# Optimization experiments

Hardware: AMD Instinct MI355X
Metric: run time of the kernel (lower is better)

## Reference

```python
import jax, jax.numpy as jnp
import numpy as np

N_NODES = 50000


def setup_inputs() -> dict:
    key = jax.random.key(0)
    ks = jax.random.split(key, 9)
    d = 256
    E = 800000
    inp = {
        "x": jax.random.normal(ks[0], (N_NODES, d), dtype=jnp.float32),
        "edge_index": jax.random.randint(ks[1], (2, E), 0, N_NODES, dtype=jnp.int64),
    }
    # 3 GCNConv layers, each: weight [in, out] and bias [out] (Glorot-ish scale)
    scale = 1.0 / np.sqrt(d)
    for i in range(3):
        inp[f"W{i+1}"] = jax.random.normal(ks[2 + 2 * i], (d, d), dtype=jnp.float32) * scale
        inp[f"b{i+1}"] = jnp.zeros((d,), dtype=jnp.float32)
    return inp


def _gcn_conv(h, src, dst, norm, W, b, n_nodes):
    # linear transform then normalized gather-scatter aggregation
    h = h @ W                                   # [N, out]
    msg = h[src] * norm[:, None]                # [E+N, out]
    out = jax.ops.segment_sum(msg, dst, num_segments=n_nodes)
    return out + b


def reference(x, edge_index, W1, b1, W2, b2, W3, b3):
    n = x.shape[0]
    loop = jnp.arange(n, dtype=edge_index.dtype)
    src = jnp.concatenate([edge_index[0], loop])  # add self-loops
    dst = jnp.concatenate([edge_index[1], loop])
    # symmetric normalization: deg^{-1/2}[src] * deg^{-1/2}[dst]
    deg = jax.ops.segment_sum(jnp.ones_like(dst, dtype=x.dtype), dst, num_segments=n)
    dinv = jnp.where(deg > 0, jax.lax.rsqrt(deg), 0.0)
    norm = dinv[src] * dinv[dst]

    h = _gcn_conv(x, src, dst, norm, W1, b1, n)
    h = jax.nn.relu(h)
    h = _gcn_conv(h, src, dst, norm, W2, b2, n)
    h = jax.nn.relu(h)
    h = _gcn_conv(h, src, dst, norm, W3, b3, n)
    return h
```

## Files before the change

kernel.cpp:

```cpp
#include <hip/hip_runtime.h>
#include <math.h>


using bf16x8  = __attribute__((ext_vector_type(8))) short;
using ushort8 = __attribute__((ext_vector_type(8))) unsigned short;
using f32x4   = __attribute__((ext_vector_type(4))) float;
using half4   = __attribute__((ext_vector_type(4))) _Float16;

__device__ inline unsigned short f2bf(float v) {
    union { float f; unsigned u; } x; x.f = v;
    unsigned r = x.u + 0x7fff + ((x.u >> 16) & 1);
    return (unsigned short)(r >> 16);
}
__device__ inline float bf2f(unsigned short b) {
    union { float f; unsigned u; } x; x.u = ((unsigned)b) << 16;
    return x.f;
}
__device__ inline unsigned short f2h_bits(float v) {
    _Float16 h = (_Float16)v;
    union { _Float16 h; unsigned short u; } c; c.h = h;
    return c.u;
}


__global__ void hist_kernel(const int* __restrict__ dst, int E, int* __restrict__ cnt) {
    int e = blockIdx.x * blockDim.x + threadIdx.x;
    if (e < E) atomicAdd(&cnt[dst[e]], 1);
}

__global__ void scan_block_kernel(const int* __restrict__ in, int n,
                                  int* __restrict__ out, int* __restrict__ bsums) {
    __shared__ int s[256];
    int t = threadIdx.x;
    int i = blockIdx.x * 256 + t;
    s[t] = (i < n) ? in[i] : 0;
    __syncthreads();
    for (int off = 1; off < 256; off <<= 1) {
        int addv = (t >= off) ? s[t - off] : 0;
        __syncthreads();
        s[t] += addv;
        __syncthreads();
    }
    if (i < n) out[i] = s[t];
    if (t == 255) bsums[blockIdx.x] = s[255];
}

__global__ void scan_sums_kernel(int* __restrict__ bsums, int nb) {
    __shared__ int s[256];
    int t = threadIdx.x;
    s[t] = (t < nb) ? bsums[t] : 0;
    __syncthreads();
    for (int off = 1; off < 256; off <<= 1) {
        int addv = (t >= off) ? s[t - off] : 0;
        __syncthreads();
        s[t] += addv;
        __syncthreads();
    }
    if (t < nb) bsums[t] = s[t];
}

__global__ void scan_add_kernel(int* __restrict__ out, int n, const int* __restrict__ bsums) {
    int i = blockIdx.x * 256 + threadIdx.x;
    if (blockIdx.x > 0 && i < n) out[i] += bsums[blockIdx.x - 1];
}

__global__ void dinv_cursor_kernel(const int* __restrict__ cnt, const int* __restrict__ scanv,
                                   float* __restrict__ dinv, int* __restrict__ cursor, int n) {
    int i = blockIdx.x * blockDim.x + threadIdx.x;
    if (i < n) {
        int c = cnt[i];
        dinv[i] = rsqrtf((float)(c + 1));
        cursor[i] = scanv[i] - c;
    }
}

__global__ void scatter_kernel(const int* __restrict__ src, const int* __restrict__ dst, int E,
                               const float* __restrict__ dinv, int* __restrict__ cursor,
                               int* __restrict__ ssrc, float* __restrict__ snorm) {
    int e = blockIdx.x * blockDim.x + threadIdx.x;
    if (e < E) {
        int s = src[e], d0 = dst[e];
        int pos = atomicAdd(&cursor[d0], 1);
        ssrc[pos] = s;
        snorm[pos] = dinv[s] * dinv[d0];
    }
}

__global__ void wsplit_kernel(const float* __restrict__ W, unsigned short* __restrict__ Wht,
                              unsigned short* __restrict__ Wlt) {
    int n = blockIdx.x;
    int k = threadIdx.x;
    float v = W[(size_t)k * 256 + n];
    unsigned short h = f2bf(v);
    unsigned short l = f2bf(v - bf2f(h));
    Wht[n * 256 + k] = h;
    Wlt[n * 256 + k] = l;
}

__global__ __launch_bounds__(256) void gemm_split_kernel(
        const float* __restrict__ A, const unsigned short* __restrict__ Bht,
        const unsigned short* __restrict__ Blt, unsigned short* __restrict__ C16, int M) {
    __shared__ unsigned short Ah[128 * 32];
    __shared__ unsigned short Al[128 * 32];
    __shared__ unsigned short Bh[128 * 32];
    __shared__ unsigned short Bl[128 * 32];

    const int tid  = threadIdx.x;
    const int lane = tid & 63;
    const int wid  = tid >> 6;
    const int wr   = wid >> 1, wc = wid & 1;
    const int mBase = blockIdx.x * 128;
    const int nBase = blockIdx.y * 128;

    const int srow = tid & 127;
    const int kseg = (tid >> 7) * 16;

    int grow = mBase + srow;
    if (grow >= M) grow = M - 1;
    const float* aptr = A + (size_t)grow * 256 + kseg;
    const unsigned short* bhbase = Bht + (size_t)(nBase + srow) * 256 + kseg;
    const unsigned short* blbase = Blt + (size_t)(nBase + srow) * 256 + kseg;

    f32x4 acc[4][4];
#pragma unroll
    for (int i = 0; i < 4; ++i)
#pragma unroll
        for (int j = 0; j < 4; ++j) acc[i][j] = (f32x4){0.f, 0.f, 0.f, 0.f};

    auto swaddr = [](int row, int k) -> int {
        int b = row * 64 + k * 2;
        return b ^ ((row & 7) << 4);
    };

    for (int k0 = 0; k0 < 256; k0 += 32) {
        float4 va[4];
        const float4* ap4 = (const float4*)(aptr + k0);
#pragma unroll
        for (int i = 0; i < 4; ++i) va[i] = ap4[i];
        ushort8 vbh[2], vbl[2];
        const ushort8* bhp = (const ushort8*)(bhbase + k0);
        const ushort8* blp = (const ushort8*)(blbase + k0);
#pragma unroll
        for (int g = 0; g < 2; ++g) { vbh[g] = bhp[g]; vbl[g] = blp[g]; }

        __syncthreads();

#pragma unroll
        for (int g = 0; g < 2; ++g) {
            float v[8];
            *(float4*)(v)     = va[2 * g];
            *(float4*)(v + 4) = va[2 * g + 1];
            ushort8 h8, l8;
#pragma unroll
            for (int j = 0; j < 8; ++j) {
                unsigned short h = f2bf(v[j]);
                h8[j] = h;
                l8[j] = f2bf(v[j] - bf2f(h));
            }
            int off = swaddr(srow, kseg + g * 8);
            *(ushort8*)((char*)Ah + off) = h8;
            *(ushort8*)((char*)Al + off) = l8;
            *(ushort8*)((char*)Bh + off) = vbh[g];
            *(ushort8*)((char*)Bl + off) = vbl[g];
        }
        __syncthreads();

        const int kb = (lane >> 4) * 8;
        bf16x8 fah[4], fal[4], fbh[4], fbl[4];
#pragma unroll
        for (int mi = 0; mi < 4; ++mi) {
            int row = wr * 64 + mi * 16 + (lane & 15);
            int off = swaddr(row, kb);
            fah[mi] = *(const bf16x8*)((const char*)Ah + off);
            fal[mi] = *(const bf16x8*)((const char*)Al + off);
        }
#pragma unroll
        for (int ni = 0; ni < 4; ++ni) {
            int col = wc * 64 + ni * 16 + (lane & 15);
            int off = swaddr(col, kb);
            fbh[ni] = *(const bf16x8*)((const char*)Bh + off);
            fbl[ni] = *(const bf16x8*)((const char*)Bl + off);
        }
#pragma unroll
        for (int mi = 0; mi < 4; ++mi)
#pragma unroll
            for (int ni = 0; ni < 4; ++ni) {
                acc[mi][ni] = __builtin_amdgcn_mfma_f32_16x16x32_bf16(
                    fah[mi], fbh[ni], acc[mi][ni], 0, 0, 0);
                acc[mi][ni] = __builtin_amdgcn_mfma_f32_16x16x32_bf16(
                    fah[mi], fbl[ni], acc[mi][ni], 0, 0, 0);
                acc[mi][ni] = __builtin_amdgcn_mfma_f32_16x16x32_bf16(
                    fal[mi], fbh[ni], acc[mi][ni], 0, 0, 0);
            }
    }

#pragma unroll
    for (int mi = 0; mi < 4; ++mi) {
        int row0 = mBase + wr * 64 + mi * 16 + (lane >> 4) * 4;
#pragma unroll
        for (int ni = 0; ni < 4; ++ni) {
            int col = nBase + wc * 64 + ni * 16 + (lane & 15);
#pragma unroll
            for (int r = 0; r < 4; ++r) {
                int row = row0 + r;
                if (row < M) C16[(size_t)row * 256 + col] = f2h_bits(acc[mi][ni][r]);
            }
        }
    }
}

template <int RELU>
__global__ __launch_bounds__(256) void agg_kernel(const unsigned short* __restrict__ hH,
                                                  const int* __restrict__ ssrc,
                                                  const float* __restrict__ snorm,
                                                  const int* __restrict__ cnt,
                                                  const int* __restrict__ scanv,
                                                  const float* __restrict__ dinv,
                                                  const float* __restrict__ bias,
                                                  float* __restrict__ out, int n) {
    int node = blockIdx.x * 4 + (threadIdx.x >> 6);
    int lane = threadIdx.x & 63;
    if (node >= n) return;
    int end = scanv[node];
    int start = end - cnt[node];
    float di = dinv[node];
    float wself = di * di;

    half4 v = ((const half4*)(hH + (size_t)node * 256))[lane];
    float ax = (float)v[0] * wself, ay = (float)v[1] * wself;
    float az = (float)v[2] * wself, aw = (float)v[3] * wself;

    int j = start;
    for (; j + 4 <= end; j += 4) {
        int s0 = ssrc[j], s1 = ssrc[j + 1], s2 = ssrc[j + 2], s3 = ssrc[j + 3];
        float w0 = snorm[j], w1 = snorm[j + 1], w2 = snorm[j + 2], w3 = snorm[j + 3];
        half4 u0 = ((const half4*)(hH + (size_t)s0 * 256))[lane];
        half4 u1 = ((const half4*)(hH + (size_t)s1 * 256))[lane];
        half4 u2 = ((const half4*)(hH + (size_t)s2 * 256))[lane];
        half4 u3 = ((const half4*)(hH + (size_t)s3 * 256))[lane];
        ax = fmaf((float)u0[0], w0, ax); ay = fmaf((float)u0[1], w0, ay);
        az = fmaf((float)u0[2], w0, az); aw = fmaf((float)u0[3], w0, aw);
        ax = fmaf((float)u1[0], w1, ax); ay = fmaf((float)u1[1], w1, ay);
        az = fmaf((float)u1[2], w1, az); aw = fmaf((float)u1[3], w1, aw);
        ax = fmaf((float)u2[0], w2, ax); ay = fmaf((float)u2[1], w2, ay);
        az = fmaf((float)u2[2], w2, az); aw = fmaf((float)u2[3], w2, aw);
        ax = fmaf((float)u3[0], w3, ax); ay = fmaf((float)u3[1], w3, ay);
        az = fmaf((float)u3[2], w3, az); aw = fmaf((float)u3[3], w3, aw);
    }
    for (; j < end; ++j) {
        int s = ssrc[j];
        float wn = snorm[j];
        half4 u = ((const half4*)(hH + (size_t)s * 256))[lane];
        ax = fmaf((float)u[0], wn, ax); ay = fmaf((float)u[1], wn, ay);
        az = fmaf((float)u[2], wn, az); aw = fmaf((float)u[3], wn, aw);
    }

    float4 bb = ((const float4*)bias)[lane];
    ax += bb.x; ay += bb.y; az += bb.z; aw += bb.w;
    if (RELU) {
        ax = fmaxf(ax, 0.0f); ay = fmaxf(ay, 0.0f);
        az = fmaxf(az, 0.0f); aw = fmaxf(aw, 0.0f);
    }
    float4 o = {ax, ay, az, aw};
    ((float4*)(out + (size_t)node * 256))[lane] = o;
}

extern "C" void kernel_launch(void* const* d_in, const int* in_sizes, int n_in,
                              void* d_out, int out_size, void* d_ws, size_t ws_size,
                              hipStream_t stream) {
    const float* x  = (const float*)d_in[0];
    const int*   ei = (const int*)d_in[1];
    const float* W1 = (const float*)d_in[2];
    const float* b1 = (const float*)d_in[3];
    const float* W2 = (const float*)d_in[4];
    const float* b2 = (const float*)d_in[5];
    const float* W3 = (const float*)d_in[6];
    const float* b3 = (const float*)d_in[7];
    float* out = (float*)d_out;

    const int n = in_sizes[0] / 256;
    const int E = in_sizes[1] / 2;
    const int* src = ei;
    const int* dst = ei + E;

    char* ws = (char*)d_ws;
    unsigned short* hH = (unsigned short*)ws;
    size_t off  = (size_t)n * 256 * 2;
    off = (off + 255) & ~(size_t)255;
    float* dinv = (float*)(ws + off); off += (size_t)n * 4;
    int*   cnt  = (int*)(ws + off);   off += (size_t)n * 4;
    int*   scn  = (int*)(ws + off);   off += (size_t)n * 4;
    int*   cur  = (int*)(ws + off);   off += (size_t)n * 4;
    int*   bsum = (int*)(ws + off);   off += 4096;
    int*   ssrc = (int*)(ws + off);   off += (size_t)E * 4;
    float* snrm = (float*)(ws + off); off += (size_t)E * 4;
    off = (off + 255) & ~(size_t)255;
    unsigned short* Wsp[6];
    for (int i = 0; i < 6; ++i) {
        Wsp[i] = (unsigned short*)(ws + off);
        off += (size_t)256 * 256 * 2;
    }

    hipMemsetAsync(cnt, 0, (size_t)n * 4, stream);

    const int eb = (E + 255) / 256;
    const int nb = (n + 255) / 256;

    wsplit_kernel<<<256, 256, 0, stream>>>(W1, Wsp[0], Wsp[1]);
    wsplit_kernel<<<256, 256, 0, stream>>>(W2, Wsp[2], Wsp[3]);
    wsplit_kernel<<<256, 256, 0, stream>>>(W3, Wsp[4], Wsp[5]);

    hist_kernel<<<eb, 256, 0, stream>>>(dst, E, cnt);
    scan_block_kernel<<<nb, 256, 0, stream>>>(cnt, n, scn, bsum);
    scan_sums_kernel<<<1, 256, 0, stream>>>(bsum, nb);
    scan_add_kernel<<<nb, 256, 0, stream>>>(scn, n, bsum);
    dinv_cursor_kernel<<<nb, 256, 0, stream>>>(cnt, scn, dinv, cur, n);
    scatter_kernel<<<eb, 256, 0, stream>>>(src, dst, E, dinv, cur, ssrc, snrm);

    dim3 gg((n + 127) / 128, 2);
    const int ab = (n + 3) / 4;

    gemm_split_kernel<<<gg, 256, 0, stream>>>(x, Wsp[0], Wsp[1], hH, n);
    agg_kernel<1><<<ab, 256, 0, stream>>>(hH, ssrc, snrm, cnt, scn, dinv, b1, out, n);
    gemm_split_kernel<<<gg, 256, 0, stream>>>(out, Wsp[2], Wsp[3], hH, n);
    agg_kernel<1><<<ab, 256, 0, stream>>>(hH, ssrc, snrm, cnt, scn, dinv, b2, out, n);
    gemm_split_kernel<<<gg, 256, 0, stream>>>(out, Wsp[4], Wsp[5], hH, n);
    agg_kernel<0><<<ab, 256, 0, stream>>>(hH, ssrc, snrm, cnt, scn, dinv, b3, out, n);
}
```

Baseline: 423.6 us.

## Pre-split activations to bf16 hi/lo and load GEMM tiles via global_load_lds

```diff
diff --git a/kernel.cpp b/kernel.cpp
--- a/kernel.cpp
+++ b/kernel.cpp
@@ -3,7 +3,7 @@
 
 
 using bf16x8  = __attribute__((ext_vector_type(8))) short;
-using ushort8 = __attribute__((ext_vector_type(8))) unsigned short;
+using ushort4v = __attribute__((ext_vector_type(4))) unsigned short;
 using f32x4   = __attribute__((ext_vector_type(4))) float;
 using half4   = __attribute__((ext_vector_type(4))) _Float16;
 
@@ -59,18 +59,16 @@
     if (t < nb) bsums[t] = s[t];
 }
 
-__global__ void scan_add_kernel(int* __restrict__ out, int n, const int* __restrict__ bsums) {
+__global__ void scan_add_dinv_kernel(int* __restrict__ scn, int n, const int* __restrict__ bsums,
+                                     const int* __restrict__ cnt, float* __restrict__ dinv,
+                                     int* __restrict__ cursor) {
     int i = blockIdx.x * 256 + threadIdx.x;
-    if (blockIdx.x > 0 && i < n) out[i] += bsums[blockIdx.x - 1];
-}
-
-__global__ void dinv_cursor_kernel(const int* __restrict__ cnt, const int* __restrict__ scanv,
-                                   float* __restrict__ dinv, int* __restrict__ cursor, int n) {
-    int i = blockIdx.x * blockDim.x + threadIdx.x;
     if (i < n) {
+        int s = scn[i] + (blockIdx.x > 0 ? bsums[blockIdx.x - 1] : 0);
+        scn[i] = s;
         int c = cnt[i];
         dinv[i] = rsqrtf((float)(c + 1));
-        cursor[i] = scanv[i] - c;
+        cursor[i] = s - c;
     }
 }
 
@@ -86,24 +84,56 @@
     }
 }
 
-__global__ void wsplit_kernel(const float* __restrict__ W, unsigned short* __restrict__ Wht,
-                              unsigned short* __restrict__ Wlt) {
-    int n = blockIdx.x;
-    int k = threadIdx.x;
-    float v = W[(size_t)k * 256 + n];
-    unsigned short h = f2bf(v);
-    unsigned short l = f2bf(v - bf2f(h));
-    Wht[n * 256 + k] = h;
-    Wlt[n * 256 + k] = l;
-}
-
-__global__ __launch_bounds__(256) void gemm_split_kernel(
-        const float* __restrict__ A, const unsigned short* __restrict__ Bht,
-        const unsigned short* __restrict__ Blt, unsigned short* __restrict__ C16, int M) {
-    __shared__ unsigned short Ah[128 * 32];
-    __shared__ unsigned short Al[128 * 32];
-    __shared__ unsigned short Bh[128 * 32];
-    __shared__ unsigned short Bl[128 * 32];
+__global__ __launch_bounds__(256) void wsplit3_kernel(const float* __restrict__ Wa,
+                                                      const float* __restrict__ Wb,
+                                                      const float* __restrict__ Wc,
+                                                      unsigned short* __restrict__ Wsp) {
+    __shared__ float t[64][65];
+    int w = blockIdx.z;
+    const float* W = (w == 0) ? Wa : (w == 1) ? Wb : Wc;
+    int k0 = blockIdx.x * 64, n0 = blockIdx.y * 64;
+    int tid = threadIdx.x;
+    int r = tid >> 6, c = tid & 63;
+#pragma unroll
+    for (int i = 0; i < 16; ++i) {
+        int kk = i * 4 + r;
+        t[kk][c] = W[(size_t)(k0 + kk) * 256 + n0 + c];
+    }
+    __syncthreads();
+    unsigned short* Hi = Wsp + (size_t)w * 131072;
+    unsigned short* Lo = Hi + 65536;
+#pragma unroll
+    for (int i = 0; i < 16; ++i) {
+        int nn = i * 4 + r;
+        float v = t[c][nn];
+        unsigned short h = f2bf(v);
+        unsigned short l2 = f2bf(v - bf2f(h));
+        Hi[(size_t)(n0 + nn) * 256 + k0 + c] = h;
+        Lo[(size_t)(n0 + nn) * 256 + k0 + c] = l2;
+    }
+}
+
+__global__ void xsplit_kernel(const float* __restrict__ in, unsigned short* __restrict__ hi,
+                              unsigned short* __restrict__ lo, int total4) {
+    int i = blockIdx.x * blockDim.x + threadIdx.x;
+    int stride = gridDim.x * blockDim.x;
+    for (; i < total4; i += stride) {
+        float4 v = ((const float4*)in)[i];
+        ushort4v h, l;
+        h[0] = f2bf(v.x); l[0] = f2bf(v.x - bf2f(h[0]));
+        h[1] = f2bf(v.y); l[1] = f2bf(v.y - bf2f(h[1]));
+        h[2] = f2bf(v.z); l[2] = f2bf(v.z - bf2f(h[2]));
+        h[3] = f2bf(v.w); l[3] = f2bf(v.w - bf2f(h[3]));
+        ((ushort4v*)hi)[i] = h;
+        ((ushort4v*)lo)[i] = l;
+    }
+}
+
+__global__ __launch_bounds__(256) void gemm_ps_kernel(
+        const unsigned short* __restrict__ Ahi, const unsigned short* __restrict__ Alo,
+        const unsigned short* __restrict__ Bht, const unsigned short* __restrict__ Blt,
+        unsigned short* __restrict__ C16, int M) {
+    __shared__ unsigned short lds[16384];
 
     const int tid  = threadIdx.x;
     const int lane = tid & 63;
@@ -112,14 +142,30 @@
     const int mBase = blockIdx.x * 128;
     const int nBase = blockIdx.y * 128;
 
-    const int srow = tid & 127;
-    const int kseg = (tid >> 7) * 16;
-
-    int grow = mBase + srow;
-    if (grow >= M) grow = M - 1;
-    const float* aptr = A + (size_t)grow * 256 + kseg;
-    const unsigned short* bhbase = Bht + (size_t)(nBase + srow) * 256 + kseg;
-    const unsigned short* blbase = Blt + (size_t)(nBase + srow) * 256 + kseg;
+    const int b0 = (lane ^ (lane >> 2) ^ (lane >> 4)) & 1;
+    const int b1 = ((lane >> 1) ^ (lane >> 3)) & 1;
+    const int b2 = ((lane >> 2) ^ (lane >> 4)) & 1;
+    const int g  = (lane & 0x38) | (b2 << 2) | (b1 << 1) | b0;
+    const int srow = g >> 2;
+    const int skg  = g & 3;
+
+    const unsigned short* gbase =
+        (wid == 0) ? Ahi : (wid == 1) ? Alo : (wid == 2) ? Bht : Blt;
+    const int rowbase = (wid < 2) ? mBase : nBase;
+
+    int grows[8];
+#pragma unroll
+    for (int c = 0; c < 8; ++c) {
+        int r = rowbase + c * 16 + srow;
+        if (wid < 2 && r >= M) r = M - 1;
+        grows[c] = r;
+    }
+    unsigned short* ldsw = lds + wid * 4096;
+
+    const unsigned short* Ah = lds;
+    const unsigned short* Al = lds + 4096;
+    const unsigned short* Bh = lds + 8192;
+    const unsigned short* Bl = lds + 12288;
 
     f32x4 acc[4][4];
 #pragma unroll
@@ -127,41 +173,14 @@
 #pragma unroll
         for (int j = 0; j < 4; ++j) acc[i][j] = (f32x4){0.f, 0.f, 0.f, 0.f};
 
-    auto swaddr = [](int row, int k) -> int {
-        int b = row * 64 + k * 2;
-        return b ^ ((row & 7) << 4);
-    };
-
     for (int k0 = 0; k0 < 256; k0 += 32) {
-        float4 va[4];
-        const float4* ap4 = (const float4*)(aptr + k0);
-#pragma unroll
-        for (int i = 0; i < 4; ++i) va[i] = ap4[i];
-        ushort8 vbh[2], vbl[2];
-        const ushort8* bhp = (const ushort8*)(bhbase + k0);
-        const ushort8* blp = (const ushort8*)(blbase + k0);
-#pragma unroll
-        for (int g = 0; g < 2; ++g) { vbh[g] = bhp[g]; vbl[g] = blp[g]; }
-
-        __syncthreads();
-
-#pragma unroll
-        for (int g = 0; g < 2; ++g) {
-            float v[8];
-            *(float4*)(v)     = va[2 * g];
-            *(float4*)(v + 4) = va[2 * g + 1];
-            ushort8 h8, l8;
-#pragma unroll
-            for (int j = 0; j < 8; ++j) {
-                unsigned short h = f2bf(v[j]);
-                h8[j] = h;
-                l8[j] = f2bf(v[j] - bf2f(h));
-            }
-            int off = swaddr(srow, kseg + g * 8);
-            *(ushort8*)((char*)Ah + off) = h8;
-            *(ushort8*)((char*)Al + off) = l8;
-            *(ushort8*)((char*)Bh + off) = vbh[g];
-            *(ushort8*)((char*)Bl + off) = vbl[g];
+#pragma unroll
+        for (int c = 0; c < 8; ++c) {
+            const unsigned short* ga = gbase + (size_t)grows[c] * 256 + k0 + skg * 8;
+            __builtin_amdgcn_global_load_lds(
+                (const __attribute__((address_space(1))) void*)ga,
+                (__attribute__((address_space(3))) void*)(ldsw + c * 512),
+                16, 0, 0);
         }
         __syncthreads();
 
@@ -170,14 +189,14 @@
 #pragma unroll
         for (int mi = 0; mi < 4; ++mi) {
             int row = wr * 64 + mi * 16 + (lane & 15);
-            int off = swaddr(row, kb);
+            int off = (row * 64 + kb * 2) ^ ((row & 7) << 4);
             fah[mi] = *(const bf16x8*)((const char*)Ah + off);
             fal[mi] = *(const bf16x8*)((const char*)Al + off);
         }
 #pragma unroll
         for (int ni = 0; ni < 4; ++ni) {
             int col = wc * 64 + ni * 16 + (lane & 15);
-            int off = swaddr(col, kb);
+            int off = (col * 64 + kb * 2) ^ ((col & 7) << 4);
             fbh[ni] = *(const bf16x8*)((const char*)Bh + off);
             fbl[ni] = *(const bf16x8*)((const char*)Bl + off);
         }
@@ -192,6 +211,7 @@
                 acc[mi][ni] = __builtin_amdgcn_mfma_f32_16x16x32_bf16(
                     fal[mi], fbh[ni], acc[mi][ni], 0, 0, 0);
             }
+        __syncthreads();
     }
 
 #pragma unroll
@@ -209,7 +229,7 @@
     }
 }
 
-template <int RELU>
+template <int RELU, int SPLIT>
 __global__ __launch_bounds__(256) void agg_kernel(const unsigned short* __restrict__ hH,
                                                   const int* __restrict__ ssrc,
                                                   const float* __restrict__ snorm,
@@ -217,7 +237,9 @@
                                                   const int* __restrict__ scanv,
                                                   const float* __restrict__ dinv,
                                                   const float* __restrict__ bias,
-                                                  float* __restrict__ out, int n) {
+                                                  unsigned short* __restrict__ outHi,
+                                                  unsigned short* __restrict__ outLo,
+                                                  float* __restrict__ outF, int n) {
     int node = blockIdx.x * 4 + (threadIdx.x >> 6);
     int lane = threadIdx.x & 63;
     if (node >= n) return;
@@ -261,8 +283,18 @@
         ax = fmaxf(ax, 0.0f); ay = fmaxf(ay, 0.0f);
         az = fmaxf(az, 0.0f); aw = fmaxf(aw, 0.0f);
     }
-    float4 o = {ax, ay, az, aw};
-    ((float4*)(out + (size_t)node * 256))[lane] = o;
+    if (SPLIT) {
+        ushort4v h, l;
+        h[0] = f2bf(ax); l[0] = f2bf(ax - bf2f(h[0]));
+        h[1] = f2bf(ay); l[1] = f2bf(ay - bf2f(h[1]));
+        h[2] = f2bf(az); l[2] = f2bf(az - bf2f(h[2]));
+        h[3] = f2bf(aw); l[3] = f2bf(aw - bf2f(h[3]));
+        ((ushort4v*)(outHi + (size_t)node * 256))[lane] = h;
+        ((ushort4v*)(outLo + (size_t)node * 256))[lane] = l;
+    } else {
+        float4 o = {ax, ay, az, aw};
+        ((float4*)(outF + (size_t)node * 256))[lane] = o;
+    }
 }
 
 extern "C" void kernel_launch(void* const* d_in, const int* in_sizes, int n_in,
@@ -276,12 +308,15 @@
     const float* b2 = (const float*)d_in[5];
     const float* W3 = (const float*)d_in[6];
     const float* b3 = (const float*)d_in[7];
-    float* out = (float*)d_out;
 
     const int n = in_sizes[0] / 256;
     const int E = in_sizes[1] / 2;
     const int* src = ei;
     const int* dst = ei + E;
+
+    unsigned short* Hi = (unsigned short*)d_out;
+    unsigned short* Lo = Hi + (size_t)n * 256;
+    float* outF = (float*)d_out;
 
     char* ws = (char*)d_ws;
     unsigned short* hH = (unsigned short*)ws;
@@ -295,35 +330,33 @@
     int*   ssrc = (int*)(ws + off);   off += (size_t)E * 4;
     float* snrm = (float*)(ws + off); off += (size_t)E * 4;
     off = (off + 255) & ~(size_t)255;
-    unsigned short* Wsp[6];
-    for (int i = 0; i < 6; ++i) {
-        Wsp[i] = (unsigned short*)(ws + off);
-        off += (size_t)256 * 256 * 2;
-    }
+    unsigned short* Wsp = (unsigned short*)(ws + off);
+    off += (size_t)3 * 2 * 65536 * 2;
 
     hipMemsetAsync(cnt, 0, (size_t)n * 4, stream);
 
     const int eb = (E + 255) / 256;
     const int nb = (n + 255) / 256;
 
-    wsplit_kernel<<<256, 256, 0, stream>>>(W1, Wsp[0], Wsp[1]);
-    wsplit_kernel<<<256, 256, 0, stream>>>(W2, Wsp[2], Wsp[3]);
-    wsplit_kernel<<<256, 256, 0, stream>>>(W3, Wsp[4], Wsp[5]);
+    wsplit3_kernel<<<dim3(4, 4, 3), 256, 0, stream>>>(W1, W2, W3, Wsp);
+    xsplit_kernel<<<2048, 256, 0, stream>>>(x, Hi, Lo, n * 64);
 
     hist_kernel<<<eb, 256, 0, stream>>>(dst, E, cnt);
     scan_block_kernel<<<nb, 256, 0, stream>>>(cnt, n, scn, bsum);
     scan_sums_kernel<<<1, 256, 0, stream>>>(bsum, nb);
-    scan_add_kernel<<<nb, 256, 0, stream>>>(scn, n, bsum);
-    dinv_cursor_kernel<<<nb, 256, 0, stream>>>(cnt, scn, dinv, cur, n);
+    scan_add_dinv_kernel<<<nb, 256, 0, stream>>>(scn, n, bsum, cnt, dinv, cur);
     scatter_kernel<<<eb, 256, 0, stream>>>(src, dst, E, dinv, cur, ssrc, snrm);
 
     dim3 gg((n + 127) / 128, 2);
     const int ab = (n + 3) / 4;
 
-    gemm_split_kernel<<<gg, 256, 0, stream>>>(x, Wsp[0], Wsp[1], hH, n);
-    agg_kernel<1><<<ab, 256, 0, stream>>>(hH, ssrc, snrm, cnt, scn, dinv, b1, out, n);
-    gemm_split_kernel<<<gg, 256, 0, stream>>>(out, Wsp[2], Wsp[3], hH, n);
-    agg_kernel<1><<<ab, 256, 0, stream>>>(hH, ssrc, snrm, cnt, scn, dinv, b2, out, n);
-    gemm_split_kernel<<<gg, 256, 0, stream>>>(out, Wsp[4], Wsp[5], hH, n);
-    agg_kernel<0><<<ab, 256, 0, stream>>>(hH, ssrc, snrm, cnt, scn, dinv, b3, out, n);
-}
+    gemm_ps_kernel<<<gg, 256, 0, stream>>>(Hi, Lo, Wsp, Wsp + 65536, hH, n);
+    agg_kernel<1, 1><<<ab, 256, 0, stream>>>(hH, ssrc, snrm, cnt, scn, dinv, b1,
+                                             Hi, Lo, nullptr, n);
+    gemm_ps_kernel<<<gg, 256, 0, stream>>>(Hi, Lo, Wsp + 131072, Wsp + 196608, hH, n);
+    agg_kernel<1, 1><<<ab, 256, 0, stream>>>(hH, ssrc, snrm, cnt, scn, dinv, b2,
+                                             Hi, Lo, nullptr, n);
+    gemm_ps_kernel<<<gg, 256, 0, stream>>>(Hi, Lo, Wsp + 262144, Wsp + 327680, hH, n);
+    agg_kernel<0, 0><<<ab, 256, 0, stream>>>(hH, ssrc, snrm, cnt, scn, dinv, b3,
+                                             nullptr, nullptr, outF, n);
+}
```

Result: faster. 398.9 us (-5.8%).
